# Kernel tuning notes

Measured on AMD Instinct MI355X. Metric: run time of the kernel, lower is better.

Reference implementation:

```python
import jax, jax.numpy as jnp
import numpy as np

HEADS = 16

def setup_inputs() -> dict:
    key = jax.random.key(0)
    ks = jax.random.split(key, 5)
    B, T, D = 2, 2048, 2048
    s = 0.02
    return {
        "x": jax.random.normal(ks[0], (B, T, D), dtype=jnp.float32),
        "Wq": jax.random.normal(ks[1], (D, D), dtype=jnp.float32) * s,
        "Wk": jax.random.normal(ks[2], (D, D), dtype=jnp.float32) * s,
        "Wv": jax.random.normal(ks[3], (D, D), dtype=jnp.float32) * s,
        "Wo": jax.random.normal(ks[4], (D, D), dtype=jnp.float32) * s,
    }

def reference(x, Wq, Wk, Wv, Wo):
    B, T, _ = x.shape
    H = HEADS
    Dh = Wq.shape[1] // H
    # projections: [B,T,H,Dh]
    q = (x @ Wq).reshape(B, T, H, Dh)
    k = (x @ Wk).reshape(B, T, H, Dh)
    v = (x @ Wv).reshape(B, T, H, Dh)
    # raw scores [B,H,T,T]
    scores = jnp.einsum("bthd,bshd->bhts", q, k)
    # NOTE (faithful to source): mask is multiplicative 0/1 tril (the
    # masked_fill(-inf) in the torch code is not in-place and has no effect),
    # and the scale is sqrt(token_len), not sqrt(head_dim).
    mask = jnp.tril(jnp.ones((T, T), dtype=scores.dtype))
    scores = scores * mask
    attn = jax.nn.softmax(scores / (T ** 0.5), axis=-1)
    out = jnp.einsum("bhts,bshd->bthd", attn, v).reshape(B, T, H * Dh)
    return out @ Wo
```

## Files before the change

### kernel.cpp

```cpp
#include <hip/hip_runtime.h>


typedef __attribute__((ext_vector_type(4))) float  f32x4;
typedef __attribute__((ext_vector_type(8))) short  bf16x8;
typedef __attribute__((ext_vector_type(4))) unsigned short u16x4;

#define AS1 __attribute__((address_space(1)))
#define AS3 __attribute__((address_space(3)))

__device__ __forceinline__ void llds16(const void* g, void* l) {
  __builtin_amdgcn_global_load_lds((const AS1 void*)g, (AS3 void*)l, 16, 0, 0);
}

__device__ __forceinline__ unsigned short f2bf(float f) {
  unsigned int u = __builtin_bit_cast(unsigned int, f);
  u += 0x7fffu + ((u >> 16) & 1u);
  return (unsigned short)(u >> 16);
}

__device__ __forceinline__ unsigned short f2bfru(float f) {
  return (unsigned short)((__builtin_bit_cast(unsigned int, f) + 0x8000u) >> 16);
}

__device__ __forceinline__ float bf2f(unsigned short u) {
  return __builtin_bit_cast(float, (unsigned int)u << 16);
}

__global__ __launch_bounds__(256) void cast_x_kernel(const float* __restrict__ in,
                                                     unsigned short* __restrict__ out) {
  int i = blockIdx.x * 256 + threadIdx.x;
  f32x4 v = ((const f32x4*)in)[i];
  u16x4 o;
  o[0] = f2bf(v[0]); o[1] = f2bf(v[1]); o[2] = f2bf(v[2]); o[3] = f2bf(v[3]);
  ((u16x4*)out)[i] = o;
}

__global__ __launch_bounds__(256) void transpose_w4_kernel(
    const float* __restrict__ W0, const float* __restrict__ W1,
    const float* __restrict__ W2, const float* __restrict__ W3,
    unsigned short* __restrict__ T0, unsigned short* __restrict__ T1,
    unsigned short* __restrict__ T2, unsigned short* __restrict__ T3) {
  __shared__ float tile[32][33];
  const int z = blockIdx.z;
  const float* W = (z == 0) ? W0 : (z == 1) ? W1 : (z == 2) ? W2 : W3;
  unsigned short* Wt = (z == 0) ? T0 : (z == 1) ? T1 : (z == 2) ? T2 : T3;
  const int bx = blockIdx.x << 5;
  const int by = blockIdx.y << 5;
  const int tx = threadIdx.x;
  const int ty = threadIdx.y;
#pragma unroll
  for (int r = ty; r < 32; r += 8)
    tile[r][tx] = W[(size_t)(bx + r) * 2048 + by + tx];
  __syncthreads();
#pragma unroll
  for (int r = ty; r < 32; r += 8)
    Wt[(size_t)(by + r) * 2048 + bx + tx] = f2bf(tile[tx][r]);
}

template <int EPI>
__global__ __launch_bounds__(512, 2) void gemm_pipe(const unsigned short* __restrict__ A,
                                                    const unsigned short* __restrict__ Bt,
                                                    unsigned short* __restrict__ Qb,
                                                    unsigned short* __restrict__ Kb,
                                                    unsigned short* __restrict__ Vt,
                                                    float* __restrict__ Co) {
  __shared__ __align__(16) char smem[98304];
  const int tid  = threadIdx.x;
  const int lane = tid & 63;
  const int w    = tid >> 6;
  const int f    = blockIdx.x;
  const int xcd  = f & 7;
  const int g    = f >> 3;
  int bm, bn;
  if constexpr (EPI == 0) { bn = xcd * 3 + (g % 3); bm = g / 3; }
  else                    { bn = xcd;              bm = g;      }
  const int wr = w >> 2, wc = w & 3;
  const int q16 = lane >> 4;
  const int l15 = lane & 15;

  const int aIdx = (w << 6) + lane;
  const int aRow = aIdx >> 2, aCph = aIdx & 3;
  const unsigned short* aSrc = A + (size_t)((bm << 7) + aRow) * 2048
                                 + ((aCph ^ ((aRow >> 1) & 3)) << 3);
  const unsigned short* bSrc0 = Bt + (size_t)((bn << 8) + aRow) * 2048
                                  + ((aCph ^ ((aRow >> 1) & 3)) << 3);
  const int bIdx1 = 512 + aIdx;
  const int bRow1 = bIdx1 >> 2, bCph1 = bIdx1 & 3;
  const unsigned short* bSrc1 = Bt + (size_t)((bn << 8) + bRow1) * 2048
                                  + ((bCph1 ^ ((bRow1 >> 1) & 3)) << 3);

  const int swx  = ((q16 ^ ((l15 >> 1) & 3)) << 4);
  const int aoff = ((wr << 6) + l15) * 64 + swx;
  const int boff = 8192 + ((wc << 6) + l15) * 64 + swx;

  f32x4 acc[4][4];
#pragma unroll
  for (int i = 0; i < 4; ++i)
#pragma unroll
    for (int j = 0; j < 4; ++j) acc[i][j] = (f32x4){0.f, 0.f, 0.f, 0.f};

  auto stageT = [&](int t, int slot) {
    char* sb = smem + slot * 24576 + (w << 10);
    const size_t ko = (size_t)t << 5;
    llds16(aSrc + ko, sb);
    llds16(bSrc0 + ko, sb + 8192);
    llds16(bSrc1 + ko, sb + 16384);
  };

  bf16x8 fa0[4], fb0[4], fa1[4], fb1[4];
  auto readFrags = [&](int slot, bf16x8* af, bf16x8* bf) {
    const char* base = smem + slot * 24576;
#pragma unroll
    for (int mi = 0; mi < 4; ++mi) af[mi] = *(const bf16x8*)(base + aoff + (mi << 10));
#pragma unroll
    for (int ni = 0; ni < 4; ++ni) bf[ni] = *(const bf16x8*)(base + boff + (ni << 10));
  };
  auto mfmaStep = [&](bf16x8* af, bf16x8* bf) {
    __builtin_amdgcn_s_setprio(1);
#pragma unroll
    for (int mi = 0; mi < 4; ++mi)
#pragma unroll
      for (int ni = 0; ni < 4; ++ni)
        acc[mi][ni] = __builtin_amdgcn_mfma_f32_16x16x32_bf16(af[mi], bf[ni], acc[mi][ni], 0, 0, 0);
    __builtin_amdgcn_s_setprio(0);
  };
  auto pipeStep = [&](int u, bf16x8* ca, bf16x8* cb, bf16x8* na, bf16x8* nb) {
    asm volatile("s_waitcnt vmcnt(3)" ::: "memory");
    asm volatile("s_barrier" ::: "memory");
    stageT(u + 3, (u + 3) & 3);
    readFrags((u + 1) & 3, na, nb);
    mfmaStep(ca, cb);
  };

  stageT(0, 0); stageT(1, 1); stageT(2, 2);
  asm volatile("s_waitcnt vmcnt(6)" ::: "memory");
  asm volatile("s_barrier" ::: "memory");
  readFrags(0, fa0, fb0);

  pipeStep(0, fa0, fb0, fa1, fb1);
#pragma unroll 1
  for (int u = 1; u < 61; u += 2) {
    pipeStep(u,     fa1, fb1, fa0, fb0);
    pipeStep(u + 1, fa0, fb0, fa1, fb1);
  }
  asm volatile("s_waitcnt vmcnt(3)" ::: "memory");
  asm volatile("s_barrier" ::: "memory");
  readFrags(2, fa0, fb0);
  mfmaStep(fa1, fb1);
  asm volatile("s_waitcnt vmcnt(0)" ::: "memory");
  asm volatile("s_barrier" ::: "memory");
  readFrags(3, fa1, fb1);
  mfmaStep(fa0, fb0);
  mfmaStep(fa1, fb1);

  const float qscale = 0.02209708691207961f;
  const int rb = q16 << 2;
#pragma unroll
  for (int mi = 0; mi < 4; ++mi) {
    int m0 = (bm << 7) + (wr << 6) + (mi << 4) + rb;
#pragma unroll
    for (int ni = 0; ni < 4; ++ni) {
      if constexpr (EPI == 0) {
        int region = bn >> 3;
        int nloc = ((bn & 7) << 8) + (wc << 6) + (ni << 4) + l15;
        if (region == 0) {
#pragma unroll
          for (int j = 0; j < 4; ++j)
            Qb[(size_t)(m0 + j) * 2048 + nloc] = f2bf(acc[mi][ni][j] * qscale);
        } else if (region == 1) {
#pragma unroll
          for (int j = 0; j < 4; ++j)
            Kb[(size_t)(m0 + j) * 2048 + nloc] = f2bf(acc[mi][ni][j]);
        } else {
          u16x4 pk;
#pragma unroll
          for (int j = 0; j < 4; ++j) pk[j] = f2bf(acc[mi][ni][j]);
          int b = m0 >> 11, t = m0 & 2047;
          *(u16x4*)(Vt + ((size_t)((b << 4) + (nloc >> 7)) * 128 + (nloc & 127)) * 2048 + t) = pk;
        }
      } else {
        int n = (bn << 8) + (wc << 6) + (ni << 4) + l15;
#pragma unroll
        for (int j = 0; j < 4; ++j)
          Co[(size_t)(m0 + j) * 2048 + n] = acc[mi][ni][j];
      }
    }
  }
}

__global__ __launch_bounds__(256) void vsuf_kernel(const unsigned short* __restrict__ Vt,
                                                   float* __restrict__ Suf) {
  const int row  = blockIdx.x * 4 + (threadIdx.x >> 6);
  const int lane = threadIdx.x & 63;
  const unsigned short* vp = Vt + (size_t)row * 2048 + (lane << 5);
  float a = 0.f;
#pragma unroll
  for (int c = 0; c < 4; ++c) {
    bf16x8 v = *(const bf16x8*)(vp + (c << 3));
#pragma unroll
    for (int j = 0; j < 8; ++j) a += bf2f((unsigned short)v[j]);
  }
  float I = a;
#pragma unroll
  for (int off = 1; off < 64; off <<= 1) {
    float t = __shfl_down(I, off, 64);
    I += (lane + off < 64) ? t : 0.f;
  }
  Suf[(size_t)lane * 4096 + row] = I;
  if (lane == 0) Suf[(size_t)64 * 4096 + row] = 0.f;
}

__global__ __launch_bounds__(256) void attn_kernel(const unsigned short* __restrict__ Q,
                                                   const unsigned short* __restrict__ K,
                                                   const unsigned short* __restrict__ V,
                                                   const float* __restrict__ Suf,
                                                   unsigned short* __restrict__ O) {
  __shared__ __align__(16) char smem[36864];
  const int tid  = threadIdx.x;
  const int lane = tid & 63;
  const int w    = tid >> 6;
  const int q16  = lane >> 4;
  const int l15  = lane & 15;
  const int f    = blockIdx.x;
  const int bh    = ((f & 7) << 2) + ((f >> 3) & 3);
  const int strip = 31 - (f >> 5);
  const int b  = bh >> 4;
  const size_t qkbase = ((size_t)(b << 11)) * 2048 + ((size_t)(bh & 15) << 7);
  const size_t vbase  = (size_t)bh << 18;
  const int rb = q16 << 2;
  char* Psm = smem + 32768 + (w << 10);

  const int numIter = 2 * strip + 2;
  const int t0 = (strip << 6) + (w << 4);

  auto stage = [&](int s0, int kb, int vb) {
#pragma unroll
    for (int c = 0; c < 2; ++c) {
      int ch = (w << 1) + c;
      int rowK = (ch << 2) + q16;
      int colbK = (l15 << 4) ^ ((rowK & 7) << 4);
      llds16(K + qkbase + (size_t)(s0 + rowK) * 2048 + (colbK >> 1), smem + kb + (ch << 10));
      int rowV = (ch << 4) + (lane >> 2);
      int colbV = ((lane & 3) << 4) ^ (((rowV >> 2) & 3) << 4);
      llds16(V + vbase + (size_t)rowV * 2048 + s0 + (colbV >> 1), smem + vb + (ch << 10));
    }
  };

  bf16x8 qf[4];
  {
    const unsigned short* qp = Q + qkbase + (size_t)(t0 + l15) * 2048 + (q16 << 3);
#pragma unroll
    for (int kk = 0; kk < 4; ++kk) qf[kk] = *(const bf16x8*)(qp + (kk << 5));
  }

  f32x4 oacc[8];
#pragma unroll
  for (int i = 0; i < 8; ++i) oacc[i] = (f32x4){0.f, 0.f, 0.f, 0.f};
  float ell[4] = {0.f, 0.f, 0.f, 0.f};

  stage(0, 0, 16384);
  asm volatile("s_waitcnt vmcnt(0)" ::: "memory");
  __syncthreads();

  int cur = 0;
  for (int it = 0; it < numIter; ++it) {
    const int s0 = it << 5;
    if (it + 1 < numIter)
      stage(s0 + 32, (cur ^ 1) << 13, 16384 + ((cur ^ 1) << 13));

    if (s0 <= t0) {
      const int kb = cur << 13;
      const int vb = 16384 + (cur << 13);

      f32x4 sA = (f32x4){0.f, 0.f, 0.f, 0.f}, sB = (f32x4){0.f, 0.f, 0.f, 0.f};
#pragma unroll
      for (int kk = 0; kk < 4; ++kk) {
        int r0 = l15;
        bf16x8 k0f = *(const bf16x8*)(smem + kb + (r0 << 8) + (((kk << 6) + (q16 << 4)) ^ ((r0 & 7) << 4)));
        sA = __builtin_amdgcn_mfma_f32_16x16x32_bf16(qf[kk], k0f, sA, 0, 0, 0);
        int r1 = 16 + l15;
        bf16x8 k1f = *(const bf16x8*)(smem + kb + (r1 << 8) + (((kk << 6) + (q16 << 4)) ^ ((r1 & 7) << 4)));
        sB = __builtin_amdgcn_mfma_f32_16x16x32_bf16(qf[kk], k1f, sB, 0, 0, 0);
      }

      float pA[4], pB[4];
      if (s0 + 31 <= t0) {
#pragma unroll
        for (int j = 0; j < 4; ++j) {
          pA[j] = __expf(sA[j]);
          pB[j] = __expf(sB[j]);
          ell[j] += pA[j] + pB[j];
        }
      } else {
#pragma unroll
        for (int j = 0; j < 4; ++j) {
          int t  = t0 + rb + j;
          int sa = s0 + l15;
          float vA = (sa <= t)      ? sA[j] : 0.f;
          float vB = (sa + 16 <= t) ? sB[j] : 0.f;
          pA[j] = __expf(vA);
          pB[j] = __expf(vB);
          ell[j] += pA[j] + pB[j];
        }
      }

#pragma unroll
      for (int j = 0; j < 4; ++j) {
        int r   = rb + j;
        int swz = ((r >> 1) & 3) << 4;
        *(unsigned short*)(Psm + (r << 6) + ((l15 << 1) ^ swz))        = f2bfru(pA[j]);
        *(unsigned short*)(Psm + (r << 6) + ((32 + (l15 << 1)) ^ swz)) = f2bfru(pB[j]);
      }
      asm volatile("s_waitcnt lgkmcnt(0)" ::: "memory");

      bf16x8 pa;
      {
        int r = l15;
        pa = *(const bf16x8*)(Psm + (r << 6) + ((q16 << 4) ^ (((r >> 1) & 3) << 4)));
      }
#pragma unroll
      for (int ni = 0; ni < 8; ++ni) {
        int dr = (ni << 4) + l15;
        bf16x8 vbf = *(const bf16x8*)(smem + vb + (dr << 6) + ((q16 << 4) ^ (((dr >> 2) & 3) << 4)));
        oacc[ni] = __builtin_amdgcn_mfma_f32_16x16x32_bf16(pa, vbf, oacc[ni], 0, 0, 0);
      }
    }

    asm volatile("s_waitcnt vmcnt(0)" ::: "memory");
    __syncthreads();
    cur ^= 1;
  }

  const int send = (t0 & ~31) + 32;
  const float* sp = Suf + (size_t)(send >> 5) * 4096 + ((size_t)bh << 7);
  const float extra = (float)(2048 - send);
#pragma unroll
  for (int ni = 0; ni < 8; ++ni) {
    float sv = sp[(ni << 4) + l15];
#pragma unroll
    for (int j = 0; j < 4; ++j) oacc[ni][j] += sv;
  }

#pragma unroll
  for (int j = 0; j < 4; ++j) {
    float r = ell[j];
    r += __shfl_xor(r, 1, 64);
    r += __shfl_xor(r, 2, 64);
    r += __shfl_xor(r, 4, 64);
    r += __shfl_xor(r, 8, 64);
    float inv = 1.0f / (r + extra);
    int t = t0 + rb + j;
    unsigned short* op = O + qkbase + (size_t)t * 2048;
#pragma unroll
    for (int ni = 0; ni < 8; ++ni)
      op[(ni << 4) + l15] = f2bf(oacc[ni][j] * inv);
  }
}

extern "C" void kernel_launch(void* const* d_in, const int* in_sizes, int n_in,
                              void* d_out, int out_size, void* d_ws, size_t ws_size,
                              hipStream_t stream) {
  (void)in_sizes; (void)n_in; (void)out_size; (void)ws_size;
  const float* x  = (const float*)d_in[0];
  const float* Wq = (const float*)d_in[1];
  const float* Wk = (const float*)d_in[2];
  const float* Wv = (const float*)d_in[3];
  const float* Wo = (const float*)d_in[4];
  float* out = (float*)d_out;

  char* ws = (char*)d_ws;
  unsigned short* Xb  = (unsigned short*)(ws);
  unsigned short* Wqt = (unsigned short*)(ws + 16777216);
  unsigned short* Wkt = (unsigned short*)(ws + 16777216 + 8388608);
  unsigned short* Wvt = (unsigned short*)(ws + 16777216 + 2 * 8388608);
  unsigned short* Wot = (unsigned short*)(ws + 16777216 + 3 * 8388608);
  unsigned short* Qb  = (unsigned short*)(ws + 50331648);
  unsigned short* Kb  = (unsigned short*)(ws + 67108864);
  unsigned short* Vt  = (unsigned short*)(ws + 83886080);
  unsigned short* Ob  = Xb;
  float*          Suf = (float*)Wqt;

  cast_x_kernel<<<8192, 256, 0, stream>>>(x, Xb);
  {
    dim3 tb(32, 8), tg(64, 64, 4);
    transpose_w4_kernel<<<tg, tb, 0, stream>>>(Wq, Wk, Wv, Wo, Wqt, Wkt, Wvt, Wot);
  }
  gemm_pipe<0><<<768, 512, 0, stream>>>(Xb, Wqt, Qb, Kb, Vt, nullptr);

  vsuf_kernel<<<1024, 256, 0, stream>>>(Vt, Suf);

  attn_kernel<<<1024, 256, 0, stream>>>(Qb, Kb, Vt, Suf, Ob);

  gemm_pipe<1><<<256, 512, 0, stream>>>(Ob, Wot, nullptr, nullptr, nullptr, out);
}
```

Baseline: 265.6 us.

## Restructure GEMM to 256-thread blocks with larger per-wave tiles and 3-slot pipeline

The GEMM kernel moves from 512 threads (8 waves, 2x4 wave grid) to 256 threads (4 waves), with each wave computing a larger output tile (8x4 MFMA tiles for the QKV projection, 4x4 for the output projection). The output projection now uses 128-wide N tiles and launches 512 blocks. The LDS pipeline drops from 4 slots with register-double-buffered fragments to 3 slots, with fragments read right before the MFMAs. The aim is more data reuse per wave and less barrier overhead, at the cost of more registers per thread, possible occupancy loss, and less LDS-read/MFMA overlap.

```diff
diff --git a/kernel.cpp b/kernel.cpp
--- a/kernel.cpp
+++ b/kernel.cpp
@@ -58,111 +58,120 @@
 }
 
 template <int EPI>
-__global__ __launch_bounds__(512, 2) void gemm_pipe(const unsigned short* __restrict__ A,
+__global__ __launch_bounds__(256, 2) void gemm_pipe(const unsigned short* __restrict__ A,
                                                     const unsigned short* __restrict__ Bt,
                                                     unsigned short* __restrict__ Qb,
                                                     unsigned short* __restrict__ Kb,
                                                     unsigned short* __restrict__ Vt,
                                                     float* __restrict__ Co) {
-  __shared__ __align__(16) char smem[98304];
+  constexpr int BN      = (EPI == 0) ? 256 : 128;
+  constexpr int MI      = (EPI == 0) ? 8 : 4;
+  constexpr int BROUNDS = BN / 64;
+  constexpr int SLOT    = 8192 + BN * 64;
+  __shared__ __align__(16) char smem[3 * SLOT];
+
   const int tid  = threadIdx.x;
   const int lane = tid & 63;
   const int w    = tid >> 6;
+  const int q16  = lane >> 4;
+  const int l15  = lane & 15;
   const int f    = blockIdx.x;
-  const int xcd  = f & 7;
   const int g    = f >> 3;
   int bm, bn;
-  if constexpr (EPI == 0) { bn = xcd * 3 + (g % 3); bm = g / 3; }
-  else                    { bn = xcd;              bm = g;      }
-  const int wr = w >> 2, wc = w & 3;
-  const int q16 = lane >> 4;
-  const int l15 = lane & 15;
-
-  const int aIdx = (w << 6) + lane;
-  const int aRow = aIdx >> 2, aCph = aIdx & 3;
-  const unsigned short* aSrc = A + (size_t)((bm << 7) + aRow) * 2048
-                                 + ((aCph ^ ((aRow >> 1) & 3)) << 3);
-  const unsigned short* bSrc0 = Bt + (size_t)((bn << 8) + aRow) * 2048
-                                  + ((aCph ^ ((aRow >> 1) & 3)) << 3);
-  const int bIdx1 = 512 + aIdx;
-  const int bRow1 = bIdx1 >> 2, bCph1 = bIdx1 & 3;
-  const unsigned short* bSrc1 = Bt + (size_t)((bn << 8) + bRow1) * 2048
-                                  + ((bCph1 ^ ((bRow1 >> 1) & 3)) << 3);
-
-  const int swx  = ((q16 ^ ((l15 >> 1) & 3)) << 4);
-  const int aoff = ((wr << 6) + l15) * 64 + swx;
-  const int boff = 8192 + ((wc << 6) + l15) * 64 + swx;
-
-  f32x4 acc[4][4];
-#pragma unroll
-  for (int i = 0; i < 4; ++i)
+  if constexpr (EPI == 0) { bn = (f & 7) * 3 + (g % 3); bm = g / 3; }
+  else                    { bn = ((f & 7) << 1) + (g & 1); bm = g >> 1; }
+  const int wmb = (EPI == 0) ? 0 : ((w >> 1) << 6);
+  const int wnb = (EPI == 0) ? (w << 6) : ((w & 1) << 6);
+
+  f32x4 acc[MI][4];
+#pragma unroll
+  for (int i = 0; i < MI; ++i)
 #pragma unroll
     for (int j = 0; j < 4; ++j) acc[i][j] = (f32x4){0.f, 0.f, 0.f, 0.f};
 
-  auto stageT = [&](int t, int slot) {
-    char* sb = smem + slot * 24576 + (w << 10);
-    const size_t ko = (size_t)t << 5;
-    llds16(aSrc + ko, sb);
-    llds16(bSrc0 + ko, sb + 8192);
-    llds16(bSrc1 + ko, sb + 16384);
+  const int rowA = tid >> 2;
+  const int chA  = tid & 3;
+  auto stageT = [&](int t, char* sb) {
+    const int k0 = t << 5;
+#pragma unroll
+    for (int r = 0; r < 2; ++r) {
+      int row = (r << 6) + rowA;
+      const unsigned short* src = A + (size_t)((bm << 7) + row) * 2048 + k0
+                                    + ((chA ^ ((row >> 1) & 3)) << 3);
+      llds16(src, sb + (r << 12) + (w << 10));
+    }
+#pragma unroll
+    for (int r = 0; r < BROUNDS; ++r) {
+      int row = (r << 6) + rowA;
+      const unsigned short* src = Bt + (size_t)(bn * BN + row) * 2048 + k0
+                                     + ((chA ^ ((row >> 1) & 3)) << 3);
+      llds16(src, sb + 8192 + (r << 12) + (w << 10));
+    }
   };
 
-  bf16x8 fa0[4], fb0[4], fa1[4], fb1[4];
-  auto readFrags = [&](int slot, bf16x8* af, bf16x8* bf) {
-    const char* base = smem + slot * 24576;
-#pragma unroll
-    for (int mi = 0; mi < 4; ++mi) af[mi] = *(const bf16x8*)(base + aoff + (mi << 10));
-#pragma unroll
-    for (int ni = 0; ni < 4; ++ni) bf[ni] = *(const bf16x8*)(base + boff + (ni << 10));
-  };
-  auto mfmaStep = [&](bf16x8* af, bf16x8* bf) {
+  auto computeT = [&](const char* base) {
+    bf16x8 af[MI], bf[4];
+#pragma unroll
+    for (int mi = 0; mi < MI; ++mi) {
+      int row = wmb + (mi << 4) + l15;
+      af[mi] = *(const bf16x8*)(base + (row << 6) + ((q16 ^ ((row >> 1) & 3)) << 4));
+    }
+#pragma unroll
+    for (int ni = 0; ni < 4; ++ni) {
+      int row = wnb + (ni << 4) + l15;
+      bf[ni] = *(const bf16x8*)(base + 8192 + (row << 6) + ((q16 ^ ((row >> 1) & 3)) << 4));
+    }
     __builtin_amdgcn_s_setprio(1);
 #pragma unroll
-    for (int mi = 0; mi < 4; ++mi)
+    for (int mi = 0; mi < MI; ++mi)
 #pragma unroll
       for (int ni = 0; ni < 4; ++ni)
         acc[mi][ni] = __builtin_amdgcn_mfma_f32_16x16x32_bf16(af[mi], bf[ni], acc[mi][ni], 0, 0, 0);
     __builtin_amdgcn_s_setprio(0);
   };
-  auto pipeStep = [&](int u, bf16x8* ca, bf16x8* cb, bf16x8* na, bf16x8* nb) {
-    asm volatile("s_waitcnt vmcnt(3)" ::: "memory");
-    asm volatile("s_barrier" ::: "memory");
-    stageT(u + 3, (u + 3) & 3);
-    readFrags((u + 1) & 3, na, nb);
-    mfmaStep(ca, cb);
+
+  auto WAITC = [&]() {
+    if constexpr (EPI == 0) asm volatile("s_waitcnt vmcnt(6)" ::: "memory");
+    else                    asm volatile("s_waitcnt vmcnt(4)" ::: "memory");
   };
-
-  stageT(0, 0); stageT(1, 1); stageT(2, 2);
-  asm volatile("s_waitcnt vmcnt(6)" ::: "memory");
-  asm volatile("s_barrier" ::: "memory");
-  readFrags(0, fa0, fb0);
-
-  pipeStep(0, fa0, fb0, fa1, fb1);
+  auto STEP = [&](int t, char* cbase, char* sbase) {
+    WAITC();
+    __builtin_amdgcn_s_barrier();
+    stageT(t + 2, sbase);
+    computeT(cbase);
+  };
+
+  char* s0 = smem;
+  char* s1 = smem + SLOT;
+  char* s2 = smem + 2 * SLOT;
+
+  stageT(0, s0); stageT(1, s1);
+
 #pragma unroll 1
-  for (int u = 1; u < 61; u += 2) {
-    pipeStep(u,     fa1, fb1, fa0, fb0);
-    pipeStep(u + 1, fa0, fb0, fa1, fb1);
-  }
-  asm volatile("s_waitcnt vmcnt(3)" ::: "memory");
-  asm volatile("s_barrier" ::: "memory");
-  readFrags(2, fa0, fb0);
-  mfmaStep(fa1, fb1);
+  for (int t = 0; t < 60; t += 3) {
+    STEP(t,     s0, s2);
+    STEP(t + 1, s1, s0);
+    STEP(t + 2, s2, s1);
+  }
+  STEP(60, s0, s2);
+  STEP(61, s1, s0);
+  WAITC();
+  __builtin_amdgcn_s_barrier();
+  computeT(s2);
   asm volatile("s_waitcnt vmcnt(0)" ::: "memory");
-  asm volatile("s_barrier" ::: "memory");
-  readFrags(3, fa1, fb1);
-  mfmaStep(fa0, fb0);
-  mfmaStep(fa1, fb1);
+  __builtin_amdgcn_s_barrier();
+  computeT(s0);
 
   const float qscale = 0.02209708691207961f;
   const int rb = q16 << 2;
 #pragma unroll
-  for (int mi = 0; mi < 4; ++mi) {
-    int m0 = (bm << 7) + (wr << 6) + (mi << 4) + rb;
+  for (int mi = 0; mi < MI; ++mi) {
+    int m0 = (bm << 7) + wmb + (mi << 4) + rb;
 #pragma unroll
     for (int ni = 0; ni < 4; ++ni) {
       if constexpr (EPI == 0) {
         int region = bn >> 3;
-        int nloc = ((bn & 7) << 8) + (wc << 6) + (ni << 4) + l15;
+        int nloc = ((bn & 7) << 8) + wnb + (ni << 4) + l15;
         if (region == 0) {
 #pragma unroll
           for (int j = 0; j < 4; ++j)
@@ -179,7 +188,7 @@
           *(u16x4*)(Vt + ((size_t)((b << 4) + (nloc >> 7)) * 128 + (nloc & 127)) * 2048 + t) = pk;
         }
       } else {
-        int n = (bn << 8) + (wc << 6) + (ni << 4) + l15;
+        int n = (bn << 7) + wnb + (ni << 4) + l15;
 #pragma unroll
         for (int j = 0; j < 4; ++j)
           Co[(size_t)(m0 + j) * 2048 + n] = acc[mi][ni][j];
@@ -385,11 +394,11 @@
     dim3 tb(32, 8), tg(64, 64, 4);
     transpose_w4_kernel<<<tg, tb, 0, stream>>>(Wq, Wk, Wv, Wo, Wqt, Wkt, Wvt, Wot);
   }
-  gemm_pipe<0><<<768, 512, 0, stream>>>(Xb, Wqt, Qb, Kb, Vt, nullptr);
+  gemm_pipe<0><<<768, 256, 0, stream>>>(Xb, Wqt, Qb, Kb, Vt, nullptr);
 
   vsuf_kernel<<<1024, 256, 0, stream>>>(Vt, Suf);
 
   attn_kernel<<<1024, 256, 0, stream>>>(Qb, Kb, Vt, Suf, Ob);
 
-  gemm_pipe<1><<<256, 512, 0, stream>>>(Ob, Wot, nullptr, nullptr, nullptr, out);
-}
+  gemm_pipe<1><<<512, 256, 0, stream>>>(Ob, Wot, nullptr, nullptr, nullptr, out);
+}
```

Measured after the change: 261.6 us. About the same (-1.5%).
